# Kernel optimization log

Hardware: AMD Instinct MI355X
Metric: run time of the kernel (lower is better)

Reference implementation:

```python
import jax, jax.numpy as jnp
import numpy as np

D = 1024   # hidden_size
H = 16     # n_head
K = 64     # head_size
B = 4
T = 1024
LAYER_ID = 12
NUM_LAYERS = 24
D_MIX = 32
D_DECAY = 64


def setup_inputs() -> dict:
    key = jax.random.key(0)
    ks = jax.random.split(key, 12)
    r01 = LAYER_ID / (NUM_LAYERS - 1)          # ratio_0_to_1
    r10 = 1.0 - LAYER_ID / NUM_LAYERS          # ratio_1_to_almost0
    ddd = jnp.arange(D, dtype=jnp.float32) / D
    maa = lambda p: (1.0 - ddd ** p).reshape(1, 1, D)
    inp = {}
    inp['x'] = jax.random.normal(ks[0], (B, T, D), jnp.float32)
    inp['time_maa_x'] = maa(r10)
    inp['time_maa_w'] = maa(r10)
    inp['time_maa_k'] = maa(r10)
    inp['time_maa_v'] = (1.0 - (ddd ** r10 + 0.3 * r01)).reshape(1, 1, D)
    inp['time_maa_r'] = maa(0.5 * r10)
    inp['time_maa_g'] = maa(0.5 * r10)
    # torch inits time_maa_w1 to zeros (trivial); use small uniform like w2 for a non-degenerate test
    inp['time_maa_w1'] = jax.random.uniform(ks[1], (D, D_MIX * 5), jnp.float32, -0.01, 0.01)
    inp['time_maa_w2'] = jax.random.uniform(ks[2], (5, D_MIX, D), jnp.float32, -0.01, 0.01)
    n = jnp.arange(D, dtype=jnp.float32)
    inp['time_decay'] = (-6.0 + 5.0 * (n / (D - 1)) ** (0.7 + 1.3 * r01)).reshape(1, 1, D)
    inp['time_decay_w1'] = jax.random.uniform(ks[3], (D, D_DECAY), jnp.float32, -0.01, 0.01)
    inp['time_decay_w2'] = jax.random.uniform(ks[4], (D_DECAY, D), jnp.float32, -0.01, 0.01)
    for nm, kk in zip(['W_r', 'W_k', 'W_v', 'W_g', 'W_o'], ks[5:10]):
        inp[nm] = jax.random.normal(kk, (D, D), jnp.float32) * 0.02
    inp['ln_w'] = jnp.ones((D,), jnp.float32)
    inp['ln_b'] = jnp.zeros((D,), jnp.float32)
    return inp


def _bidir_shift(x):
    # (x[i-1] + x[i+1]) / 2 with zero padding at the boundaries
    left = jnp.pad(x[:, :-1, :], ((0, 0), (1, 0), (0, 0)))
    right = jnp.pad(x[:, 1:, :], ((0, 0), (0, 1), (0, 0)))
    return 0.5 * (left + right)


def _lion_attention(r, k, v, w):
    # r,k,v,w: (B,H,T,Khd), w = -exp(decay) <= 0
    Tn = r.shape[2]
    cs = jnp.cumsum(w, axis=2)
    cs_b = cs - w
    shift_f = cs[:, :, Tn // 2:Tn // 2 + 1, :]
    shift_b = cs_b[:, :, Tn // 2:Tn // 2 + 1, :]
    cf = jnp.clip(cs - shift_f, -60.0, 60.0)
    cb = jnp.clip(cs_b - shift_b, -60.0, 60.0)
    # A_fwd = tril(Q*e^{cf} @ (K*e^{-cf})^T); A_bwd = triu(Q*e^{-cb} @ (K*e^{cb})^T, 1)
    A_f = jnp.einsum('bhik,bhjk->bhij', r * jnp.exp(cf), k * jnp.exp(-cf))
    A_b = jnp.einsum('bhik,bhjk->bhij', r * jnp.exp(-cb), k * jnp.exp(cb))
    idx = jnp.arange(Tn)
    lower = idx[:, None] >= idx[None, :]   # tril incl. diagonal
    A = jnp.where(lower, A_f, A_b)         # == tril(A_f) + triu(A_b, 1)
    return jnp.einsum('bhij,bhjk->bhik', A, v)


def reference(x, time_maa_x, time_maa_w, time_maa_k, time_maa_v, time_maa_r, time_maa_g,
              time_maa_w1, time_maa_w2, time_decay, time_decay_w1, time_decay_w2,
              W_r, W_k, W_v, W_g, W_o, ln_w, ln_b):
    Bn, Tn, Dn = x.shape
    Hh, Kk = H, Dn // H
    dxprev = _bidir_shift(x) - x
    # data-dependent token-shift mixing coefficients (LoRA-style)
    xxx = jnp.tanh((x + dxprev * time_maa_x) @ time_maa_w1)          # (B,T,5*32)
    mm = jnp.einsum('btfm,fmd->fbtd', xxx.reshape(Bn, Tn, 5, D_MIX), time_maa_w2)
    mw, mk, mv, mr, mg = mm[0], mm[1], mm[2], mm[3], mm[4]
    xw = x + dxprev * (time_maa_w + mw)
    xk = x + dxprev * (time_maa_k + mk)
    xv = x + dxprev * (time_maa_v + mv)
    xr = x + dxprev * (time_maa_r + mr)
    xg = x + dxprev * (time_maa_g + mg)
    r = xr @ W_r.T
    k = xk @ W_k.T
    v = xv @ W_v.T
    g = jax.nn.silu(xg @ W_g.T)
    w = time_decay + jnp.tanh(xw @ time_decay_w1) @ time_decay_w2   # (B,T,D)
    to_h = lambda t: t.reshape(Bn, Tn, Hh, Kk).transpose(0, 2, 1, 3)
    y = _lion_attention(to_h(r), to_h(k), to_h(v), -jnp.exp(to_h(w)))
    y = y.transpose(0, 2, 1, 3).reshape(Bn * Tn, Dn)
    # GroupNorm(n_head groups, eps = 1e-5 * head_size_divisor^2)
    eps = 1e-5 * 64.0
    yg = y.reshape(Bn * Tn, Hh, Kk)
    mu = jnp.mean(yg, axis=-1, keepdims=True)
    var = jnp.var(yg, axis=-1, keepdims=True)
    yn = ((yg - mu) * jax.lax.rsqrt(var + eps)).reshape(Bn * Tn, Dn) * ln_w + ln_b
    y = yn.reshape(Bn, Tn, Dn)
    return (y * g) @ W_o.T
```

## Files before the change

### kernel.cpp

```cpp
#include <hip/hip_runtime.h>
#include <math.h>

#define NB 4
#define TT 1024
#define DD 1024
#define NTOK 4096
#define ND (NTOK*DD)

typedef __attribute__((ext_vector_type(8))) short bh8;
typedef __attribute__((ext_vector_type(4))) float fx4;

__device__ __forceinline__ unsigned short f2bf(float f) {
    unsigned int b = __float_as_uint(f);
    b += 0x7fffu + ((b >> 16) & 1u);
    return (unsigned short)(b >> 16);
}

__device__ __forceinline__ unsigned pkbf(float a, float b) {
#if __has_builtin(__builtin_amdgcn_cvt_pk_bf16_f32)
    auto r = __builtin_amdgcn_cvt_pk_bf16_f32(a, b);
    unsigned u;
    __builtin_memcpy(&u, &r, 4);
    return u;
#else
    return ((unsigned)f2bf(b) << 16) | f2bf(a);
#endif
}

#define GLD16(gp, lp) __builtin_amdgcn_global_load_lds( \
    (__attribute__((address_space(1))) void*)(gp), \
    (__attribute__((address_space(3))) void*)(lp), 16, 0, 0)

__global__ __launch_bounds__(256) void k_prep(const float* __restrict__ W_r, const float* __restrict__ W_k,
                                              const float* __restrict__ W_v, const float* __restrict__ W_g,
                                              const float* __restrict__ W_o,
                                              const float* __restrict__ w1, const float* __restrict__ dw1,
                                              const float* __restrict__ w2,
                                              unsigned short* __restrict__ Wrb, unsigned short* __restrict__ Wkb,
                                              unsigned short* __restrict__ Wvb, unsigned short* __restrict__ Wgb,
                                              unsigned short* __restrict__ Wob,
                                              unsigned short* __restrict__ w1T, unsigned short* __restrict__ dw1T,
                                              unsigned short* __restrict__ w2T16) {
    int y = blockIdx.y, bx = blockIdx.x, tid = threadIdx.x;
    if (y < 5) {
        if (bx >= 512) return;
        const float* s = (y == 0) ? W_r : (y == 1) ? W_k : (y == 2) ? W_v : (y == 3) ? W_g : W_o;
        unsigned short* d = (y == 0) ? Wrb : (y == 1) ? Wkb : (y == 2) ? Wvb : (y == 3) ? Wgb : Wob;
        int i = (bx * 256 + tid) * 8;
        float4 a = *(const float4*)(s + i);
        float4 b = *(const float4*)(s + i + 4);
        uint4 o;
        o.x = pkbf(a.x, a.y);
        o.y = pkbf(a.z, a.w);
        o.z = pkbf(b.x, b.y);
        o.w = pkbf(b.z, b.w);
        *(uint4*)(d + i) = o;
    } else if (y == 5) {
        int o = bx * 256 + tid;
        int r = o & 1023, c = o >> 10;
        w1T[o] = f2bf(w1[r * 160 + c]);
    } else {
        if (bx < 256) {
            int o = bx * 256 + tid;
            int r = o & 1023, c = o >> 10;
            dw1T[o] = f2bf(dw1[r * 64 + c]);
        } else if (bx < 276) {
            int wi = bx - 256;
            int f = wi >> 2;
            int d = (wi & 3) * 256 + tid;
#pragma unroll 8
            for (int m = 0; m < 32; m++)
                w2T16[(size_t)(f * 1024 + d) * 32 + m] = f2bf(w2[(size_t)(f * 32 + m) * 1024 + d]);
        }
    }
}

__global__ __launch_bounds__(256) void k_mixx(const float* __restrict__ x,
                                              const float* __restrict__ maa_x,
                                              unsigned short* __restrict__ xmix16) {
    int base = (blockIdx.x * 256 + threadIdx.x) * 4;
    int t = (base >> 10) & 1023;
    int d = base & 1023;
    float4 xv = *(const float4*)(x + base);
    float4 xm = (t > 0)    ? *(const float4*)(x + base - 1024) : make_float4(0, 0, 0, 0);
// ... 150 lines not shown
    for (int c = 0; c < 4; c++) {
        int d = c * 256 + tid;
        float acc[8] = {};
#pragma unroll 8
        for (int j = 0; j < 64; j++) {
            float wv = dw2[j * 1024 + d];
#pragma unroll
            for (int g = 0; g < 8; g++) acc[g] = fmaf(hl[g][j], wv, acc[g]);
        }
        float td = tdec[d];
#pragma unroll
        for (int g = 0; g < 8; g++) ew[(tok0 + g) * 1024 + d] = -expf(td + acc[g]);
    }
}

__global__ __launch_bounds__(64) void k_scan1(const float* __restrict__ ew, float* __restrict__ segsum) {
    int bx = blockIdx.x;
    int b = bx >> 9, seg = (bx >> 4) & 31, dch = bx & 15;
    int d = dch * 64 + threadIdx.x;
    size_t base = ((size_t)(b * 1024 + seg * 32)) * 1024 + d;
    float s = 0.f;
#pragma unroll 8
    for (int t = 0; t < 32; t++) s += ew[base + (size_t)t * 1024];
    segsum[(b * 32 + seg) * 1024 + d] = s;
}

__global__ __launch_bounds__(64) void k_scan3(const float* __restrict__ ew, const float* __restrict__ segsum,
                                              float* __restrict__ cf, float* __restrict__ cb) {
    int bx = blockIdx.x;
    int b = bx >> 9, seg = (bx >> 4) & 31, dch = bx & 15;
    int d = dch * 64 + threadIdx.x;
    float run = 0.f, pre = 0.f, off16 = 0.f;
#pragma unroll
    for (int s = 0; s < 32; s++) {
        float tv = segsum[(b * 32 + s) * 1024 + d];
        if (s == seg) pre = run;
        if (s == 16) off16 = run;
        run += tv;
    }
    float e512 = ew[((size_t)(b * 1024 + 512)) * 1024 + d];
    float sb = off16;
    float sf = off16 + e512;
    float cum = pre;
    size_t base = ((size_t)(b * 1024 + seg * 32)) * 1024 + d;
#pragma unroll 4
    for (int t = 0; t < 32; t++) {
        float prev = cum;
        cum += ew[base + (size_t)t * 1024];
        cf[base + (size_t)t * 1024] = fminf(fmaxf(cum - sf, -60.f), 60.f);
        cb[base + (size_t)t * 1024] = fminf(fmaxf(prev - sb, -60.f), 60.f);
    }
}

__device__ __forceinline__ void gemm_body(const unsigned short* __restrict__ A,
                                          const unsigned short* __restrict__ W,
                                          int m0, int n0, int mode,
                                          float* __restrict__ Cf,
                                          unsigned short* __restrict__ O1,
                                          unsigned short* __restrict__ O2,
                                          const float* __restrict__ cfp,
                                          const float* __restrict__ cbp,
                                          char* smem) {
    int tid = threadIdx.x;
    int w = tid >> 6, lane = tid & 63, l15 = lane & 15, qd = lane >> 4;
    int wm = w >> 1, wn = w & 1;
    fx4 acc[4][4];
#pragma unroll
    for (int mt = 0; mt < 4; mt++)
#pragma unroll
        for (int nt = 0; nt < 4; nt++)
#pragma unroll
            for (int r = 0; r < 4; r++) acc[mt][nt][r] = 0.f;
    unsigned short* sA = (unsigned short*)smem;
    unsigned short* sB = (unsigned short*)(smem + 8192);
    int rowA = tid >> 2, cA = tid & 3;
    for (int kb = 0; kb < 1024; kb += 32) {
        __syncthreads();
        GLD16(A + (size_t)(m0 + rowA) * 1024 + kb + cA * 8,      sA + w * 512);
        GLD16(A + (size_t)(m0 + 64 + rowA) * 1024 + kb + cA * 8, sA + 2048 + w * 512);
        GLD16(W + (size_t)(n0 + rowA) * 1024 + kb + cA * 8,      sB + w * 512);
        GLD16(W + (size_t)(n0 + 64 + rowA) * 1024 + kb + cA * 8, sB + 2048 + w * 512);
        __syncthreads();
        bh8 af[4], bfr[4];
#pragma unroll
        for (int mt = 0; mt < 4; mt++)
            af[mt] = *(const bh8*)(sA + (wm * 64 + mt * 16 + l15) * 32 + qd * 8);
#pragma unroll
        for (int nt = 0; nt < 4; nt++)
            bfr[nt] = *(const bh8*)(sB + (wn * 64 + nt * 16 + l15) * 32 + qd * 8);
#pragma unroll
        for (int mt = 0; mt < 4; mt++)
#pragma unroll
            for (int nt = 0; nt < 4; nt++)
                acc[mt][nt] = __builtin_amdgcn_mfma_f32_16x16x32_bf16(af[mt], bfr[nt], acc[mt][nt], 0, 0, 0);
    }
    int mb = m0 + wm * 64, nb = n0 + wn * 64;
    if (mode <= 1) {
#pragma unroll
        for (int mt = 0; mt < 4; mt++)
#pragma unroll
            for (int nt = 0; nt < 4; nt++) {
                fx4 s = acc[mt][nt];
#pragma unroll
                for (int r = 0; r < 4; r++) {
                    float v = s[r];
                    if (mode == 1) v = v / (1.f + __expf(-v));
                    Cf[(size_t)(mb + mt * 16 + qd * 4 + r) * 1024 + nb + nt * 16 + l15] = v;
                }
            }
    } else if (mode <= 3) {
        float s1 = (mode == 2) ? 1.f : -1.f;
#pragma unroll
        for (int mt = 0; mt < 4; mt++)
#pragma unroll
            for (int nt = 0; nt < 4; nt++) {
                fx4 s = acc[mt][nt];
#pragma unroll
                for (int r = 0; r < 4; r++) {
                    size_t idx = (size_t)(mb + mt * 16 + qd * 4 + r) * 1024 + nb + nt * 16 + l15;
                    float v = s[r];
                    O1[idx] = f2bf(v * __expf(s1 * cfp[idx]));
                    O2[idx] = f2bf(v * __expf(-s1 * cbp[idx]));
                }
            }
    } else {
        __syncthreads();
        unsigned short* T = (unsigned short*)smem;
#pragma unroll
        for (int mt = 0; mt < 4; mt++)
#pragma unroll
            for (int nt = 0; nt < 4; nt++) {
                fx4 s = acc[mt][nt];
                int dl = wn * 64 + nt * 16 + l15;
                int tl = wm * 64 + mt * 16 + qd * 4;
                uint2 pk;
                pk.x = pkbf(s[0], s[1]);
                pk.y = pkbf(s[2], s[3]);
                *(uint2*)(T + dl * 136 + tl) = pk;
            }
        __syncthreads();
        int dl = tid >> 1, hf = tid & 1;
        int bq = m0 >> 10, t0 = m0 & 1023;
#pragma unroll
        for (int i = 0; i < 8; i++) {
            uint4 vv4 = *(const uint4*)(T + dl * 136 + hf * 64 + i * 8);
            *(uint4*)(O1 + (size_t)(bq * 1024 + n0 + dl) * 1024 + t0 + hf * 64 + i * 8) = vv4;
        }
    }
}

__global__ __launch_bounds__(256, 2) void k_gemm4(const unsigned short* __restrict__ xr16,
                                                  const unsigned short* __restrict__ xk16,
                                                  const unsigned short* __restrict__ xv16,
                                                  const unsigned short* __restrict__ xg16,
                                                  const unsigned short* __restrict__ Wrb,
                                                  const unsigned short* __restrict__ Wkb,
                                                  const unsigned short* __restrict__ Wvb,
                                                  const unsigned short* __restrict__ Wgb,
                                                  unsigned short* __restrict__ qf, unsigned short* __restrict__ qb,
                                                  unsigned short* __restrict__ kf, unsigned short* __restrict__ kb,
                                                  unsigned short* __restrict__ vvt,
                                                  float* __restrict__ gg,
                                                  const float* __restrict__ cf, const float* __restrict__ cb) {
    __shared__ __align__(16) char smem[34816];
    int m0 = (blockIdx.x >> 3) * 128, n0 = (blockIdx.x & 7) * 128;
    int y = blockIdx.y;
    if (y == 0)      gemm_body(xr16, Wrb, m0, n0, 2, nullptr, qf, qb, cf, cb, smem);
    else if (y == 1) gemm_body(xk16, Wkb, m0, n0, 3, nullptr, kf, kb, cf, cb, smem);
    else if (y == 2) gemm_body(xv16, Wvb, m0, n0, 4, nullptr, vvt, nullptr, nullptr, nullptr, smem);
    else             gemm_body(xg16, Wgb, m0, n0, 1, gg, nullptr, nullptr, nullptr, nullptr, smem);
}

__global__ __launch_bounds__(256, 2) void k_gemmo(const unsigned short* __restrict__ z16,
                                                  const unsigned short* __restrict__ Wob,
                                                  float* __restrict__ out) {
    __shared__ __align__(16) char smem[34816];
    gemm_body(z16, Wob, (blockIdx.x >> 3) * 128, (blockIdx.x & 7) * 128, 0, out,
              nullptr, nullptr, nullptr, nullptr, smem);
}

__global__ __launch_bounds__(256, 2) void k_attn(const unsigned short* __restrict__ qf,
                                                 const unsigned short* __restrict__ qb,
                                                 const unsigned short* __restrict__ kf,
                                                 const unsigned short* __restrict__ kb,
                                                 const unsigned short* __restrict__ vvt,
                                                 float* __restrict__ y) {
    __shared__ __align__(16) char smem[16384];
    unsigned short* sK = (unsigned short*)smem;
    unsigned short* sV = (unsigned short*)(smem + 8192);
    int tid = threadIdx.x;
    int w = tid >> 6, lane = tid & 63, l15 = lane & 15, qd = lane >> 4;
    int bid = blockIdx.x;
    int bh = (bid & 7) + ((bid >> 6) << 3);
    int ib = (bid >> 3) & 7;
    int b = bh >> 4, h = bh & 15;
    int i0w = ib * 128 + w * 32;
    int bt0 = b * 1024;
    const unsigned short* vrow = vvt + (size_t)(b * 1024 + h * 64 + w * 16 + l15) * 1024 + qd * 8;
    int fmax = (i0w + 31) >> 6;
    int bmin = i0w >> 6;
    int srcA = l15 + ((lane & 16) << 1);
    int srcB = srcA + 16;
    fx4 yacc[4][2];
#pragma unroll
    for (int mt = 0; mt < 4; mt++)
#pragma unroll
        for (int nt = 0; nt < 2; nt++)
#pragma unroll
            for (int r = 0; r < 4; r++) yacc[mt][nt][r] = 0.f;

    for (int phase = 0; phase < 2; phase++) {
        const unsigned short* Q = phase ? qb : qf;
        const unsigned short* K = phase ? kb : kf;
        bh8 qfr[2][2];
#pragma unroll
        for (int nt = 0; nt < 2; nt++)
#pragma unroll
            for (int ks = 0; ks < 2; ks++)
                qfr[nt][ks] = *(const bh8*)(Q + (size_t)(bt0 + i0w + nt * 16 + l15) * 1024
                                              + h * 64 + ks * 32 + qd * 8);
        int jlo = phase == 0 ? 0 : 2 * ib;
        int jhi = phase == 0 ? 2 * ib + 1 : 15;
        const unsigned short* krow = K + (size_t)(bt0 + w * 16 + l15) * 1024 + h * 64 + qd * 8;
        for (int jt = jlo; jt <= jhi; jt++) {
            int jb = jt * 64;
            __syncthreads();
            GLD16(krow + (size_t)jb * 1024,        sK + w * 512);
            GLD16(krow + (size_t)jb * 1024 + 32,   sK + 2048 + w * 512);
            GLD16(vrow + jb,                        sV + w * 512);
            GLD16(vrow + jb + 32,                   sV + 2048 + w * 512);
            __syncthreads();
// ... 116 lines not shown
    const float* dw1   = (const float*)d_in[10];
    const float* dw2   = (const float*)d_in[11];
    const float* W_r   = (const float*)d_in[12];
    const float* W_k   = (const float*)d_in[13];
    const float* W_v   = (const float*)d_in[14];
    const float* W_g   = (const float*)d_in[15];
    const float* W_o   = (const float*)d_in[16];
    const float* lnw   = (const float*)d_in[17];
    const float* lnb   = (const float*)d_in[18];

    float* ws = (float*)d_ws;
    size_t o = 0;
    float* dech   = ws + o; o += 262144;
    float* segsum = ws + o; o += 131072;
    float* ew     = ws + o; o += 4194304;
    float* cf     = ws + o; o += 4194304;
    float* cb     = ws + o; o += 4194304;
    float* gg     = ws + o; o += 4194304;
    unsigned short* us = (unsigned short*)(ws + o);
    size_t u = 0;
    unsigned short* xmix16 = us + u; u += 4194304;
    unsigned short* xw16 = us + u; u += 4194304;
    unsigned short* xr16 = us + u; u += 4194304;
    unsigned short* xk16 = us + u; u += 4194304;
    unsigned short* xv16 = us + u; u += 4194304;
    unsigned short* xg16 = us + u; u += 4194304;
    unsigned short* qf   = us + u; u += 4194304;
    unsigned short* qb   = us + u; u += 4194304;
    unsigned short* kf   = us + u; u += 4194304;
    unsigned short* kb   = us + u; u += 4194304;
    unsigned short* vvt  = us + u; u += 4194304;
    unsigned short* Wrb  = us + u; u += 1048576;
    unsigned short* Wkb  = us + u; u += 1048576;
    unsigned short* Wvb  = us + u; u += 1048576;
    unsigned short* Wgb  = us + u; u += 1048576;
    unsigned short* Wob  = us + u; u += 1048576;
    unsigned short* w1T  = us + u; u += 163840;
    unsigned short* dw1T = us + u; u += 65536;
    unsigned short* xxx16 = us + u; u += 655360;
    unsigned short* w2T16 = us + u; u += 163840;
    float* yb0 = cf;
    unsigned short* z16 = xr16;

    k_prep<<<dim3(640, 7), 256, 0, stream>>>(W_r, W_k, W_v, W_g, W_o, w1, dw1, w2,
                                             Wrb, Wkb, Wvb, Wgb, Wob, w1T, dw1T, w2T16);
    k_mixx<<<4096, 256, 0, stream>>>(x, maa_x, xmix16);
    k_xxx2<<<256, 64, 0, stream>>>(xmix16, w1T, xxx16);
    k_mmix<<<dim3(16, 32), 256, 0, stream>>>(x, xxx16, w2T16, maa_w, maa_k, maa_v, maa_r, maa_g,
                                             xw16, xk16, xv16, xr16, xg16);
    k_dec1m<<<256, 64, 0, stream>>>(xw16, dw1T, dech);
    k_dec2<<<512, 256, 0, stream>>>(dech, dw2, tdec, ew);
    k_scan1<<<2048, 64, 0, stream>>>(ew, segsum);
    k_scan3<<<2048, 64, 0, stream>>>(ew, segsum, cf, cb);
    k_gemm4<<<dim3(256, 4), 256, 0, stream>>>(xr16, xk16, xv16, xg16, Wrb, Wkb, Wvb, Wgb,
                                              qf, qb, kf, kb, vvt, gg, cf, cb);
    k_attn<<<512, 256, 0, stream>>>(qf, qb, kf, kb, vvt, yb0);
    k_gn<<<16384, 256, 0, stream>>>(yb0, gg, lnw, lnb, z16);
    k_gemmo<<<256, 256, 0, stream>>>(z16, Wob, (float*)d_out);
}
```

Before: 344.8 us.

## Replace QKVG GEMM with 256x256-tile double-buffered 512-thread pipelined kernel

Replaces the 128x128-tile four-way GEMM for r/k/v/g projections with a new kernel using 256x256 tiles, 512 threads, and 128KB of LDS double-buffered via direct global-to-LDS loads. The K loop is split into phases that interleave async loads with MFMA bursts under raised wave priority, with an XCD-aware block remap. It aims to raise arithmetic intensity and overlap memory with compute. The cost is lower occupancy, since 128KB of LDS allows one block per CU despite the launch bound, and a more fragile hand-tuned waitcnt schedule.

```diff
diff --git a/kernel.cpp b/kernel.cpp
--- a/kernel.cpp
+++ b/kernel.cpp
@@ -30,6 +30,8 @@
 #define GLD16(gp, lp) __builtin_amdgcn_global_load_lds( \
     (__attribute__((address_space(1))) void*)(gp), \
     (__attribute__((address_space(3))) void*)(lp), 16, 0, 0)
+
+#define BARF() do { __builtin_amdgcn_s_barrier(); asm volatile("" ::: "memory"); } while (0)
 
 __global__ __launch_bounds__(256) void k_prep(const float* __restrict__ W_r, const float* __restrict__ W_k,
                                               const float* __restrict__ W_v, const float* __restrict__ W_g,
@@ -383,26 +385,176 @@
     }
 }
 
-__global__ __launch_bounds__(256, 2) void k_gemm4(const unsigned short* __restrict__ xr16,
-                                                  const unsigned short* __restrict__ xk16,
-                                                  const unsigned short* __restrict__ xv16,
-                                                  const unsigned short* __restrict__ xg16,
-                                                  const unsigned short* __restrict__ Wrb,
-                                                  const unsigned short* __restrict__ Wkb,
-                                                  const unsigned short* __restrict__ Wvb,
-                                                  const unsigned short* __restrict__ Wgb,
-                                                  unsigned short* __restrict__ qf, unsigned short* __restrict__ qb,
-                                                  unsigned short* __restrict__ kf, unsigned short* __restrict__ kb,
-                                                  unsigned short* __restrict__ vvt,
-                                                  float* __restrict__ gg,
-                                                  const float* __restrict__ cf, const float* __restrict__ cb) {
-    __shared__ __align__(16) char smem[34816];
-    int m0 = (blockIdx.x >> 3) * 128, n0 = (blockIdx.x & 7) * 128;
-    int y = blockIdx.y;
-    if (y == 0)      gemm_body(xr16, Wrb, m0, n0, 2, nullptr, qf, qb, cf, cb, smem);
-    else if (y == 1) gemm_body(xk16, Wkb, m0, n0, 3, nullptr, kf, kb, cf, cb, smem);
-    else if (y == 2) gemm_body(xv16, Wvb, m0, n0, 4, nullptr, vvt, nullptr, nullptr, nullptr, smem);
-    else             gemm_body(xg16, Wgb, m0, n0, 1, gg, nullptr, nullptr, nullptr, nullptr, smem);
+
+#define STA(dstbuf, g, kbv, Apt) GLD16(Apt + (size_t)(m0 + aBase + (g) * 32 + lr) * 1024 + (kbv) + swz, \
+                                       (dstbuf) + (aBase + (g) * 32) * 64)
+#define STB(dstbuf, s, kbv, Wpt) GLD16(Wpt + (size_t)(n0 + bBase + (s) * 64 + lr) * 1024 + (kbv) + swz, \
+                                       (dstbuf) + (bBase + (s) * 64) * 64)
+
+#define PHASE(mt0_, STAGE_, TAIL_) do {                                                  \
+    bh8 aA0 = *(const bh8*)(sAc + arA + (mt0_) * 1024 + fc0);                            \
+    bh8 aA1 = *(const bh8*)(sAc + arA + (mt0_) * 1024 + fc1);                            \
+    bh8 aB0 = *(const bh8*)(sAc + arA + ((mt0_) + 1) * 1024 + fc0);                      \
+    bh8 aB1 = *(const bh8*)(sAc + arA + ((mt0_) + 1) * 1024 + fc1);                      \
+    STAGE_;                                                                              \
+    BARF();                                                                              \
+    asm volatile("s_waitcnt lgkmcnt(0)" ::: "memory");                                   \
+    __builtin_amdgcn_s_setprio(1);                                                       \
+    _Pragma("unroll")                                                                    \
+    for (int nt = 0; nt < 4; ++nt) {                                                     \
+        acc[(mt0_)][nt]     = __builtin_amdgcn_mfma_f32_16x16x32_bf16(aA0, bfr[nt][0], acc[(mt0_)][nt], 0, 0, 0);     \
+        acc[(mt0_)][nt]     = __builtin_amdgcn_mfma_f32_16x16x32_bf16(aA1, bfr[nt][1], acc[(mt0_)][nt], 0, 0, 0);     \
+        acc[(mt0_) + 1][nt] = __builtin_amdgcn_mfma_f32_16x16x32_bf16(aB0, bfr[nt][0], acc[(mt0_) + 1][nt], 0, 0, 0); \
+        acc[(mt0_) + 1][nt] = __builtin_amdgcn_mfma_f32_16x16x32_bf16(aB1, bfr[nt][1], acc[(mt0_) + 1][nt], 0, 0, 0); \
+    }                                                                                    \
+    __builtin_amdgcn_s_setprio(0);                                                       \
+    TAIL_;                                                                               \
+    BARF();                                                                              \
+} while (0)
+
+__global__ __launch_bounds__(512, 2) void k_qkvg(const unsigned short* __restrict__ xr16,
+                                                 const unsigned short* __restrict__ xk16,
+                                                 const unsigned short* __restrict__ xv16,
+                                                 const unsigned short* __restrict__ xg16,
+                                                 const unsigned short* __restrict__ Wrb,
+                                                 const unsigned short* __restrict__ Wkb,
+                                                 const unsigned short* __restrict__ Wvb,
+                                                 const unsigned short* __restrict__ Wgb,
+                                                 unsigned short* __restrict__ qf, unsigned short* __restrict__ qb,
+                                                 unsigned short* __restrict__ kf, unsigned short* __restrict__ kb,
+                                                 unsigned short* __restrict__ vvt,
+                                                 float* __restrict__ gg,
+                                                 const float* __restrict__ cf, const float* __restrict__ cb) {
+    __shared__ __align__(16) char smem[131072];
+    unsigned short* sA0 = (unsigned short*)smem;
+    unsigned short* sB0 = (unsigned short*)(smem + 32768);
+    unsigned short* sA1 = (unsigned short*)(smem + 65536);
+    unsigned short* sB1 = (unsigned short*)(smem + 98304);
+
+    int flat = blockIdx.x;
+    int wk = (flat & 7) * 32 + (flat >> 3);
+    int gy = wk >> 6;
+    int wi = wk & 63;
+    int m0 = (wi >> 2) * 256, n0 = (wi & 3) * 256;
+
+    const unsigned short* Ap = (gy == 0) ? xr16 : (gy == 1) ? xk16 : (gy == 2) ? xv16 : xg16;
+    const unsigned short* Wp = (gy == 0) ? Wrb : (gy == 1) ? Wkb : (gy == 2) ? Wvb : Wgb;
+
+    int tid = threadIdx.x;
+    int lane = tid & 63, w = tid >> 6;
+    int l15 = lane & 15, qd = lane >> 4;
+    int wm = w >> 2, wn = w & 3;
+    int lr = lane >> 3;
+    int swz = ((lane & 7) ^ lr) << 3;
+    int aBase = wm * 128 + (w & 3) * 8;
+    int bBase = w * 8;
+    int fc0 = (qd * 8) ^ ((l15 & 7) << 3);
+    int fc1 = fc0 ^ 32;
+    int arA = (wm * 128 + l15) * 64;
+    int arB = (wn * 64 + l15) * 64;
+
+    fx4 acc[8][4];
+#pragma unroll
+    for (int mt = 0; mt < 8; mt++)
+#pragma unroll
+        for (int nt = 0; nt < 4; nt++)
+#pragma unroll
+            for (int r = 0; r < 4; r++) acc[mt][nt][r] = 0.f;
+
+#pragma unroll
+    for (int g = 0; g < 4; ++g) STA(sA0, g, 0, Ap);
+#pragma unroll
+    for (int s = 0; s < 4; ++s) STB(sB0, s, 0, Wp);
+    asm volatile("" ::: "memory");
+#pragma unroll
+    for (int s = 0; s < 4; ++s) STB(sB1, s, 64, Wp);
+    STA(sA1, 0, 64, Ap);
+    STA(sA1, 1, 64, Ap);
+    asm volatile("s_waitcnt vmcnt(6)" ::: "memory");
+    BARF();
+
+    unsigned short* sAc = sA0;
+    unsigned short* sBc = sB0;
+    unsigned short* sAn = sA1;
+    unsigned short* sBn = sB1;
+
+#pragma unroll 1
+    for (int t = 0; t < 16; ++t) {
+        int kb1 = t * 64 + 64, kb2 = t * 64 + 128;
+        bh8 bfr[4][2];
+#pragma unroll
+        for (int nt = 0; nt < 4; ++nt) {
+            bfr[nt][0] = *(const bh8*)(sBc + arB + nt * 1024 + fc0);
+            bfr[nt][1] = *(const bh8*)(sBc + arB + nt * 1024 + fc1);
+        }
+        PHASE(0, if (t < 15) { STA(sAn, 2, kb1, Ap); STA(sAn, 3, kb1, Ap); }, );
+        PHASE(2, if (t < 14) { STB(sBc, 0, kb2, Wp); STB(sBc, 1, kb2, Wp); }, );
+        PHASE(4, if (t < 14) { STB(sBc, 2, kb2, Wp); STB(sBc, 3, kb2, Wp); }, );
+        PHASE(6, if (t < 14) { STA(sAc, 0, kb2, Ap); STA(sAc, 1, kb2, Ap); },
+                 if (t < 14) { asm volatile("s_waitcnt vmcnt(6)" ::: "memory"); }
+                 else if (t == 14) { asm volatile("s_waitcnt vmcnt(0)" ::: "memory"); } );
+        unsigned short* tp;
+        tp = sAc; sAc = sAn; sAn = tp;
+        tp = sBc; sBc = sBn; sBn = tp;
+    }
+
+    int mb = m0 + wm * 128, nb = n0 + wn * 64;
+    if (gy == 3) {
+#pragma unroll
+        for (int mt = 0; mt < 8; mt++)
+#pragma unroll
+            for (int nt = 0; nt < 4; nt++)
+#pragma unroll
+                for (int r = 0; r < 4; r++) {
+                    float v = acc[mt][nt][r];
+                    v = v / (1.f + __expf(-v));
+                    gg[(size_t)(mb + mt * 16 + qd * 4 + r) * 1024 + nb + nt * 16 + l15] = v;
+                }
+    } else if (gy == 2) {
+        __syncthreads();
+        unsigned short* T = (unsigned short*)smem;
+        int bq = m0 >> 10, t0 = m0 & 1023;
+#pragma unroll 1
+        for (int h = 0; h < 2; ++h) {
+            if (wm == h) {
+#pragma unroll
+                for (int mt = 0; mt < 8; mt++)
+#pragma unroll
+                    for (int nt = 0; nt < 4; nt++) {
+                        int dl = wn * 64 + nt * 16 + l15;
+                        int rl = mt * 16 + qd * 4;
+                        uint2 pk;
+                        pk.x = pkbf(acc[mt][nt][0], acc[mt][nt][1]);
+                        pk.y = pkbf(acc[mt][nt][2], acc[mt][nt][3]);
+                        *(uint2*)(T + dl * 136 + rl) = pk;
+                    }
+            }
+            __syncthreads();
+#pragma unroll
+            for (int i = 0; i < 8; ++i) {
+                int gch = i * 512 + tid;
+                int d = gch >> 4, tch = gch & 15;
+                uint4 vv = *(const uint4*)(T + d * 136 + tch * 8);
+                *(uint4*)(vvt + (size_t)(bq * 1024 + n0 + d) * 1024 + t0 + h * 128 + tch * 8) = vv;
+            }
+            __syncthreads();
+        }
+    } else {
+        unsigned short* O1 = gy ? kf : qf;
+        unsigned short* O2 = gy ? kb : qb;
+        float s1 = gy ? -1.f : 1.f;
+#pragma unroll
+        for (int mt = 0; mt < 8; mt++)
+#pragma unroll
+            for (int nt = 0; nt < 4; nt++)
+#pragma unroll
+                for (int r = 0; r < 4; r++) {
+                    size_t idx = (size_t)(mb + mt * 16 + qd * 4 + r) * 1024 + nb + nt * 16 + l15;
+                    float v = acc[mt][nt][r];
+                    O1[idx] = f2bf(v * __expf(s1 * cf[idx]));
+                    O2[idx] = f2bf(v * __expf(-s1 * cb[idx]));
+                }
+    }
 }
 
 __global__ __launch_bounds__(256, 2) void k_gemmo(const unsigned short* __restrict__ z16,
@@ -633,8 +785,8 @@
     k_dec2<<<512, 256, 0, stream>>>(dech, dw2, tdec, ew);
     k_scan1<<<2048, 64, 0, stream>>>(ew, segsum);
     k_scan3<<<2048, 64, 0, stream>>>(ew, segsum, cf, cb);
-    k_gemm4<<<dim3(256, 4), 256, 0, stream>>>(xr16, xk16, xv16, xg16, Wrb, Wkb, Wvb, Wgb,
-                                              qf, qb, kf, kb, vvt, gg, cf, cb);
+    k_qkvg<<<dim3(256), dim3(512), 0, stream>>>(xr16, xk16, xv16, xg16, Wrb, Wkb, Wvb, Wgb,
+                                                qf, qb, kf, kb, vvt, gg, cf, cb);
     k_attn<<<512, 256, 0, stream>>>(qf, qb, kf, kb, vvt, yb0);
     k_gn<<<16384, 256, 0, stream>>>(yb0, gg, lnw, lnb, z16);
     k_gemmo<<<256, 256, 0, stream>>>(z16, Wob, (float*)d_out);
```

Measured after the change: 343.7 us. Within noise of the previous version (-0.3%).

## Replace QKVG GEMM with 128x256-tile, 512-thread, triple-buffered direct-to-LDS kernel

Applied to the files above, without the earlier changes.

The four projection GEMMs move from the shared gemm_body (128x128 tiles, 256 threads) to a dedicated kernel with 128x256 tiles, 8 waves, and a three-stage global_load_lds pipeline using explicit vmcnt waits and raw barriers. Block indices are remapped so that consecutive blocks are spread across XCDs. MFMA sections are wrapped in s_setprio. The epilogues for silu, the decay-scaled q/k outputs and the transposed v are rewritten to fit the new tiling. The goal is more reuse per loaded tile and better overlap of memory with compute, at the cost of a 72KB LDS footprint per block that limits occupancy.

```diff
diff --git a/kernel.cpp b/kernel.cpp
--- a/kernel.cpp
+++ b/kernel.cpp
@@ -30,6 +30,8 @@
 #define GLD16(gp, lp) __builtin_amdgcn_global_load_lds( \
     (__attribute__((address_space(1))) void*)(gp), \
     (__attribute__((address_space(3))) void*)(lp), 16, 0, 0)
+
+#define BARF() do { __builtin_amdgcn_s_barrier(); asm volatile("" ::: "memory"); } while (0)
 
 __global__ __launch_bounds__(256) void k_prep(const float* __restrict__ W_r, const float* __restrict__ W_k,
                                               const float* __restrict__ W_v, const float* __restrict__ W_g,
@@ -383,26 +385,155 @@
     }
 }
 
-__global__ __launch_bounds__(256, 2) void k_gemm4(const unsigned short* __restrict__ xr16,
-                                                  const unsigned short* __restrict__ xk16,
-                                                  const unsigned short* __restrict__ xv16,
-                                                  const unsigned short* __restrict__ xg16,
-                                                  const unsigned short* __restrict__ Wrb,
-                                                  const unsigned short* __restrict__ Wkb,
-                                                  const unsigned short* __restrict__ Wvb,
-                                                  const unsigned short* __restrict__ Wgb,
-                                                  unsigned short* __restrict__ qf, unsigned short* __restrict__ qb,
-                                                  unsigned short* __restrict__ kf, unsigned short* __restrict__ kb,
-                                                  unsigned short* __restrict__ vvt,
-                                                  float* __restrict__ gg,
-                                                  const float* __restrict__ cf, const float* __restrict__ cb) {
-    __shared__ __align__(16) char smem[34816];
-    int m0 = (blockIdx.x >> 3) * 128, n0 = (blockIdx.x & 7) * 128;
-    int y = blockIdx.y;
-    if (y == 0)      gemm_body(xr16, Wrb, m0, n0, 2, nullptr, qf, qb, cf, cb, smem);
-    else if (y == 1) gemm_body(xk16, Wkb, m0, n0, 3, nullptr, kf, kb, cf, cb, smem);
-    else if (y == 2) gemm_body(xv16, Wvb, m0, n0, 4, nullptr, vvt, nullptr, nullptr, nullptr, smem);
-    else             gemm_body(xg16, Wgb, m0, n0, 1, gg, nullptr, nullptr, nullptr, nullptr, smem);
+__global__ __launch_bounds__(512, 2) void k_qkvg(const unsigned short* __restrict__ xr16,
+                                                 const unsigned short* __restrict__ xk16,
+                                                 const unsigned short* __restrict__ xv16,
+                                                 const unsigned short* __restrict__ xg16,
+                                                 const unsigned short* __restrict__ Wrb,
+                                                 const unsigned short* __restrict__ Wkb,
+                                                 const unsigned short* __restrict__ Wvb,
+                                                 const unsigned short* __restrict__ Wgb,
+                                                 unsigned short* __restrict__ qf, unsigned short* __restrict__ qb,
+                                                 unsigned short* __restrict__ kf, unsigned short* __restrict__ kb,
+                                                 unsigned short* __restrict__ vvt,
+                                                 float* __restrict__ gg,
+                                                 const float* __restrict__ cf, const float* __restrict__ cb) {
+    __shared__ __align__(16) char smem[73728];
+    int flat = blockIdx.x;
+    int wk = (flat & 7) * 64 + (flat >> 3);
+    int gy = wk >> 7;
+    int rem = wk & 127;
+    int m0 = (rem >> 2) * 128, n0 = (rem & 3) * 256;
+
+    const unsigned short* Ap = (gy == 0) ? xr16 : (gy == 1) ? xk16 : (gy == 2) ? xv16 : xg16;
+    const unsigned short* Wp = (gy == 0) ? Wrb : (gy == 1) ? Wkb : (gy == 2) ? Wvb : Wgb;
+
+    int tid = threadIdx.x;
+    int lane = tid & 63, w = tid >> 6;
+    int l15 = lane & 15, qd = lane >> 4;
+    int wm = w >> 2, wn = w & 3;
+
+    int lrow = lane >> 2, lblk = lane & 3;
+    int gblk = lblk ^ (lrow & 3);
+    const unsigned short* agp  = Ap + (size_t)(m0 + w * 16 + lrow) * 1024 + gblk * 8;
+    const unsigned short* bgp0 = Wp + (size_t)(n0 + w * 16 + lrow) * 1024 + gblk * 8;
+    const unsigned short* bgp1 = Wp + (size_t)(n0 + 128 + w * 16 + lrow) * 1024 + gblk * 8;
+
+    unsigned short* pa0 = (unsigned short*)smem;
+    unsigned short* pa1 = pa0 + 4096;
+    unsigned short* pa2 = pa0 + 8192;
+    unsigned short* pb0 = (unsigned short*)(smem + 24576);
+    unsigned short* pb1 = pb0 + 8192;
+    unsigned short* pb2 = pb0 + 16384;
+
+    int acb = (qd ^ (l15 & 3)) * 8;
+    int arow = (wm * 64 + l15) * 32;
+    int brow = (wn * 64 + l15) * 32;
+
+#define QSTAGE(pa, pb, kbv) do { \
+    GLD16(agp + (kbv),  (pa) + w * 512); \
+    GLD16(bgp0 + (kbv), (pb) + w * 512); \
+    GLD16(bgp1 + (kbv), (pb) + 4096 + w * 512); \
+} while (0)
+
+    fx4 acc[4][4];
+#pragma unroll
+    for (int mt = 0; mt < 4; mt++)
+#pragma unroll
+        for (int nt = 0; nt < 4; nt++)
+#pragma unroll
+            for (int r = 0; r < 4; r++) acc[mt][nt][r] = 0.f;
+
+    QSTAGE(pa0, pb0, 0);
+    QSTAGE(pa1, pb1, 32);
+    asm volatile("s_waitcnt vmcnt(3)" ::: "memory");
+    BARF();
+
+    unsigned short *pac = pa0, *pan = pa1, *pap = pa2;
+    unsigned short *pbc = pb0, *pbn = pb1, *pbp = pb2;
+
+#pragma unroll 1
+    for (int t = 0; t < 32; ++t) {
+        bh8 a[4], b[4];
+#pragma unroll
+        for (int mt = 0; mt < 4; ++mt) a[mt] = *(const bh8*)(pac + arow + mt * 512 + acb);
+#pragma unroll
+        for (int nt = 0; nt < 4; ++nt) b[nt] = *(const bh8*)(pbc + brow + nt * 512 + acb);
+        if (t < 30) QSTAGE(pap, pbp, (t + 2) * 32);
+        __builtin_amdgcn_s_setprio(1);
+#pragma unroll
+        for (int nt = 0; nt < 4; ++nt)
+#pragma unroll
+            for (int mt = 0; mt < 4; ++mt)
+                acc[mt][nt] = __builtin_amdgcn_mfma_f32_16x16x32_bf16(a[mt], b[nt], acc[mt][nt], 0, 0, 0);
+        __builtin_amdgcn_s_setprio(0);
+        if (t < 30)      asm volatile("s_waitcnt vmcnt(3)" ::: "memory");
+        else if (t == 30) asm volatile("s_waitcnt vmcnt(0)" ::: "memory");
+        BARF();
+        unsigned short* tp;
+        tp = pac; pac = pan; pan = pap; pap = tp;
+        tp = pbc; pbc = pbn; pbn = pbp; pbp = tp;
+    }
+#undef QSTAGE
+
+    int mb = m0 + wm * 64, nb = n0 + wn * 64;
+    if (gy == 3) {
+#pragma unroll
+        for (int mt = 0; mt < 4; mt++)
+#pragma unroll
+            for (int nt = 0; nt < 4; nt++)
+#pragma unroll
+                for (int r = 0; r < 4; r++) {
+                    float v = acc[mt][nt][r];
+                    v = v / (1.f + __expf(-v));
+                    gg[(size_t)(mb + mt * 16 + qd * 4 + r) * 1024 + nb + nt * 16 + l15] = v;
+                }
+    } else if (gy == 2) {
+        __syncthreads();
+        unsigned short* T = (unsigned short*)smem;
+        int bq = m0 >> 10, t0 = m0 & 1023;
+#pragma unroll 1
+        for (int h = 0; h < 2; ++h) {
+            if ((wn >> 1) == h) {
+#pragma unroll
+                for (int mt = 0; mt < 4; mt++)
+#pragma unroll
+                    for (int nt = 0; nt < 4; nt++) {
+                        int dl = (wn & 1) * 64 + nt * 16 + l15;
+                        int tl = wm * 64 + mt * 16 + qd * 4;
+                        uint2 pk;
+                        pk.x = pkbf(acc[mt][nt][0], acc[mt][nt][1]);
+                        pk.y = pkbf(acc[mt][nt][2], acc[mt][nt][3]);
+                        *(uint2*)(T + dl * 136 + tl) = pk;
+                    }
+            }
+            __syncthreads();
+            {
+                int r = tid >> 2, seg = tid & 3;
+#pragma unroll
+                for (int i = 0; i < 4; ++i) {
+                    uint4 vv = *(const uint4*)(T + r * 136 + seg * 32 + i * 8);
+                    *(uint4*)(vvt + (size_t)(bq * 1024 + n0 + 128 * h + r) * 1024 + t0 + seg * 32 + i * 8) = vv;
+                }
+            }
+            __syncthreads();
+        }
+    } else {
+        unsigned short* O1 = gy ? kf : qf;
+        unsigned short* O2 = gy ? kb : qb;
+        float s1 = gy ? -1.f : 1.f;
+#pragma unroll
+        for (int mt = 0; mt < 4; mt++)
+#pragma unroll
+            for (int nt = 0; nt < 4; nt++)
+#pragma unroll
+                for (int r = 0; r < 4; r++) {
+                    size_t idx = (size_t)(mb + mt * 16 + qd * 4 + r) * 1024 + nb + nt * 16 + l15;
+                    float v = acc[mt][nt][r];
+                    O1[idx] = f2bf(v * __expf(s1 * cf[idx]));
+                    O2[idx] = f2bf(v * __expf(-s1 * cb[idx]));
+                }
+    }
 }
 
 __global__ __launch_bounds__(256, 2) void k_gemmo(const unsigned short* __restrict__ z16,
@@ -633,8 +764,8 @@
     k_dec2<<<512, 256, 0, stream>>>(dech, dw2, tdec, ew);
     k_scan1<<<2048, 64, 0, stream>>>(ew, segsum);
     k_scan3<<<2048, 64, 0, stream>>>(ew, segsum, cf, cb);
-    k_gemm4<<<dim3(256, 4), 256, 0, stream>>>(xr16, xk16, xv16, xg16, Wrb, Wkb, Wvb, Wgb,
-                                              qf, qb, kf, kb, vvt, gg, cf, cb);
+    k_qkvg<<<dim3(512), dim3(512), 0, stream>>>(xr16, xk16, xv16, xg16, Wrb, Wkb, Wvb, Wgb,
+                                                qf, qb, kf, kb, vvt, gg, cf, cb);
     k_attn<<<512, 256, 0, stream>>>(qf, qb, kf, kb, vvt, yb0);
     k_gn<<<16384, 256, 0, stream>>>(yb0, gg, lnw, lnb, z16);
     k_gemmo<<<256, 256, 0, stream>>>(z16, Wob, (float*)d_out);
```

Result: no change. 347.2 us (+0.7%).

## Rewrite projection GEMMs with split-K waves, triple-buffered LDS and swizzled tiles

Applied to the files above, without the earlier changes.

Replaces the 128x128 single-buffered GEMM body with a 256x128 tile computed by 8 waves. The waves split K into two halves and reduce their partial sums through LDS. K-tiles of 64 are triple-buffered with direct global-to-LDS loads, manual vmcnt waits and XOR-swizzled layouts, and MFMA priority is raised, all to overlap loads with compute and avoid bank conflicts. Block indices are remapped for L2 locality. The cost is large LDS use (144KB), which limits occupancy to one block per CU, plus an extra reduction pass, and the V-transpose epilogue now runs in two halves.

```diff
diff --git a/kernel.cpp b/kernel.cpp
--- a/kernel.cpp
+++ b/kernel.cpp
@@ -30,6 +30,8 @@
 #define GLD16(gp, lp) __builtin_amdgcn_global_load_lds( \
     (__attribute__((address_space(1))) void*)(gp), \
     (__attribute__((address_space(3))) void*)(lp), 16, 0, 0)
+
+#define BARF() do { __builtin_amdgcn_s_barrier(); asm volatile("" ::: "memory"); } while (0)
 
 __global__ __launch_bounds__(256) void k_prep(const float* __restrict__ W_r, const float* __restrict__ W_k,
                                               const float* __restrict__ W_v, const float* __restrict__ W_g,
@@ -286,131 +288,218 @@
     }
 }
 
-__device__ __forceinline__ void gemm_body(const unsigned short* __restrict__ A,
-                                          const unsigned short* __restrict__ W,
-                                          int m0, int n0, int mode,
-                                          float* __restrict__ Cf,
-                                          unsigned short* __restrict__ O1,
-                                          unsigned short* __restrict__ O2,
-                                          const float* __restrict__ cfp,
-                                          const float* __restrict__ cbp,
-                                          char* smem) {
+#define QST(slotoff, kbv) do { \
+    unsigned short* _sa = (unsigned short*)(smem + (slotoff)); \
+    unsigned short* _sb = _sa + 16384; \
+    GLD16(aSrc + (kbv),         _sa + (w * 32) * 64); \
+    GLD16(aSrc + 8192 + (kbv),  _sa + (w * 32 + 8) * 64); \
+    GLD16(aSrc + 16384 + (kbv), _sa + (w * 32 + 16) * 64); \
+    GLD16(aSrc + 24576 + (kbv), _sa + (w * 32 + 24) * 64); \
+    GLD16(bSrc + (kbv),         _sb + (w * 16) * 64); \
+    GLD16(bSrc + 8192 + (kbv),  _sb + (w * 16 + 8) * 64); \
+} while (0)
+
+__device__ __forceinline__ void gemm_k2(const unsigned short* __restrict__ A,
+                                        const unsigned short* __restrict__ W,
+                                        int m0, int n0, int mode,
+                                        float* __restrict__ Cf,
+                                        unsigned short* __restrict__ O1,
+                                        unsigned short* __restrict__ O2,
+                                        const float* __restrict__ cfp,
+                                        const float* __restrict__ cbp,
+                                        char* smem) {
     int tid = threadIdx.x;
-    int w = tid >> 6, lane = tid & 63, l15 = lane & 15, qd = lane >> 4;
-    int wm = w >> 1, wn = w & 1;
-    fx4 acc[4][4];
-#pragma unroll
-    for (int mt = 0; mt < 4; mt++)
+    int lane = tid & 63, w = tid >> 6;
+    int l15 = lane & 15, qd = lane >> 4;
+    int wk = w >> 2, wm = (w >> 1) & 1, wn = w & 1;
+    int lr = lane >> 3, lb = lane & 7;
+    int gblk = lb ^ lr;
+    const unsigned short* aSrc = A + (size_t)(m0 + w * 32 + lr) * 1024 + gblk * 8;
+    const unsigned short* bSrc = W + (size_t)(n0 + w * 16 + lr) * 1024 + gblk * 8;
+    int fc = ((wk * 4 + qd) ^ (l15 & 7)) * 8;
+    int arow = (wm * 128 + l15) * 64 + fc;
+    int brow = (wn * 64 + l15) * 64 + fc;
+
+    fx4 acc[8][4];
+#pragma unroll
+    for (int mt = 0; mt < 8; mt++)
 #pragma unroll
         for (int nt = 0; nt < 4; nt++)
 #pragma unroll
             for (int r = 0; r < 4; r++) acc[mt][nt][r] = 0.f;
-    unsigned short* sA = (unsigned short*)smem;
-    unsigned short* sB = (unsigned short*)(smem + 8192);
-    int rowA = tid >> 2, cA = tid & 3;
-    for (int kb = 0; kb < 1024; kb += 32) {
-        __syncthreads();
-        GLD16(A + (size_t)(m0 + rowA) * 1024 + kb + cA * 8,      sA + w * 512);
-        GLD16(A + (size_t)(m0 + 64 + rowA) * 1024 + kb + cA * 8, sA + 2048 + w * 512);
-        GLD16(W + (size_t)(n0 + rowA) * 1024 + kb + cA * 8,      sB + w * 512);
-        GLD16(W + (size_t)(n0 + 64 + rowA) * 1024 + kb + cA * 8, sB + 2048 + w * 512);
-        __syncthreads();
-        bh8 af[4], bfr[4];
-#pragma unroll
-        for (int mt = 0; mt < 4; mt++)
-            af[mt] = *(const bh8*)(sA + (wm * 64 + mt * 16 + l15) * 32 + qd * 8);
-#pragma unroll
-        for (int nt = 0; nt < 4; nt++)
-            bfr[nt] = *(const bh8*)(sB + (wn * 64 + nt * 16 + l15) * 32 + qd * 8);
-#pragma unroll
-        for (int mt = 0; mt < 4; mt++)
-#pragma unroll
-            for (int nt = 0; nt < 4; nt++)
-                acc[mt][nt] = __builtin_amdgcn_mfma_f32_16x16x32_bf16(af[mt], bfr[nt], acc[mt][nt], 0, 0, 0);
-    }
-    int mb = m0 + wm * 64, nb = n0 + wn * 64;
-    if (mode <= 1) {
-#pragma unroll
-        for (int mt = 0; mt < 4; mt++)
-#pragma unroll
-            for (int nt = 0; nt < 4; nt++) {
-                fx4 s = acc[mt][nt];
-#pragma unroll
-                for (int r = 0; r < 4; r++) {
-                    float v = s[r];
-                    if (mode == 1) v = v / (1.f + __expf(-v));
-                    Cf[(size_t)(mb + mt * 16 + qd * 4 + r) * 1024 + nb + nt * 16 + l15] = v;
-                }
-            }
-    } else if (mode <= 3) {
-        float s1 = (mode == 2) ? 1.f : -1.f;
-#pragma unroll
-        for (int mt = 0; mt < 4; mt++)
-#pragma unroll
-            for (int nt = 0; nt < 4; nt++) {
-                fx4 s = acc[mt][nt];
-#pragma unroll
-                for (int r = 0; r < 4; r++) {
-                    size_t idx = (size_t)(mb + mt * 16 + qd * 4 + r) * 1024 + nb + nt * 16 + l15;
-                    float v = s[r];
-                    O1[idx] = f2bf(v * __expf(s1 * cfp[idx]));
-                    O2[idx] = f2bf(v * __expf(-s1 * cbp[idx]));
-                }
+
+    QST(0, 0);
+    QST(49152, 64);
+    asm volatile("s_waitcnt vmcnt(6)" ::: "memory");
+    BARF();
+
+    int oc = 0, on = 49152, o2 = 98304;
+#pragma unroll 1
+    for (int t = 0; t < 16; ++t) {
+        if (t < 14) QST(o2, (t + 2) * 64);
+        const unsigned short* cA = (const unsigned short*)(smem + oc);
+        const unsigned short* cB = cA + 16384;
+        bh8 a[8], b[4];
+#pragma unroll
+        for (int mt = 0; mt < 8; ++mt) a[mt] = *(const bh8*)(cA + arow + mt * 1024);
+#pragma unroll
+        for (int nt = 0; nt < 4; ++nt) b[nt] = *(const bh8*)(cB + brow + nt * 1024);
+        __builtin_amdgcn_s_setprio(1);
+#pragma unroll
+        for (int nt = 0; nt < 4; ++nt)
+#pragma unroll
+            for (int mt = 0; mt < 8; ++mt)
+                acc[mt][nt] = __builtin_amdgcn_mfma_f32_16x16x32_bf16(a[mt], b[nt], acc[mt][nt], 0, 0, 0);
+        __builtin_amdgcn_s_setprio(0);
+        asm volatile("s_waitcnt lgkmcnt(0)" ::: "memory");
+        if (t < 14)       asm volatile("s_waitcnt vmcnt(6)" ::: "memory");
+        else if (t == 14) asm volatile("s_waitcnt vmcnt(0)" ::: "memory");
+        BARF();
+        int tmp = oc; oc = on; on = o2; o2 = tmp;
+    }
+
+    float* R = (float*)smem;
+    float* rb = R + (wm * 2 + wn) * 8192 + lane * 4;
+    if (wk == 1) {
+#pragma unroll
+        for (int mi = 0; mi < 4; ++mi)
+#pragma unroll
+            for (int nt = 0; nt < 4; ++nt)
+                *(fx4*)(rb + (mi * 4 + nt) * 256) = acc[mi][nt];
+    } else {
+#pragma unroll
+        for (int mi = 0; mi < 4; ++mi)
+#pragma unroll
+            for (int nt = 0; nt < 4; ++nt)
+                *(fx4*)(rb + (16 + mi * 4 + nt) * 256) = acc[mi + 4][nt];
+    }
+    asm volatile("s_waitcnt lgkmcnt(0)" ::: "memory");
+    BARF();
+    if (wk == 0) {
+#pragma unroll
+        for (int mi = 0; mi < 4; ++mi)
+#pragma unroll
+            for (int nt = 0; nt < 4; ++nt) {
+                fx4 v = *(const fx4*)(rb + (mi * 4 + nt) * 256);
+                acc[mi][nt] = acc[mi][nt] + v;
             }
     } else {
-        __syncthreads();
+#pragma unroll
+        for (int mi = 0; mi < 4; ++mi)
+#pragma unroll
+            for (int nt = 0; nt < 4; ++nt) {
+                fx4 v = *(const fx4*)(rb + (16 + mi * 4 + nt) * 256);
+                acc[mi + 4][nt] = acc[mi + 4][nt] + v;
+            }
+    }
+    asm volatile("s_waitcnt lgkmcnt(0)" ::: "memory");
+    BARF();
+
+    int mbase = m0 + wm * 128;
+    int nb = n0 + wn * 64;
+#define EPI(AOFF) do { \
+    if (mode <= 1) { \
+        _Pragma("unroll") \
+        for (int mi = 0; mi < 4; ++mi) \
+        { _Pragma("unroll") \
+          for (int nt = 0; nt < 4; ++nt) \
+          { _Pragma("unroll") \
+            for (int r = 0; r < 4; ++r) { \
+                float v = acc[mi + AOFF][nt][r]; \
+                if (mode == 1) v = v / (1.f + __expf(-v)); \
+                Cf[(size_t)(mbase + (mi + AOFF) * 16 + qd * 4 + r) * 1024 + nb + nt * 16 + l15] = v; \
+            } } } \
+    } else if (mode <= 3) { \
+        float s1 = (mode == 2) ? 1.f : -1.f; \
+        _Pragma("unroll") \
+        for (int mi = 0; mi < 4; ++mi) \
+        { _Pragma("unroll") \
+          for (int nt = 0; nt < 4; ++nt) \
+          { _Pragma("unroll") \
+            for (int r = 0; r < 4; ++r) { \
+                size_t idx = (size_t)(mbase + (mi + AOFF) * 16 + qd * 4 + r) * 1024 + nb + nt * 16 + l15; \
+                float v = acc[mi + AOFF][nt][r]; \
+                O1[idx] = f2bf(v * __expf(s1 * cfp[idx])); \
+                O2[idx] = f2bf(v * __expf(-s1 * cbp[idx])); \
+            } } } \
+    } \
+} while (0)
+    if (mode != 4) {
+        if (wk == 0) EPI(0); else EPI(4);
+    } else {
         unsigned short* T = (unsigned short*)smem;
-#pragma unroll
-        for (int mt = 0; mt < 4; mt++)
-#pragma unroll
-            for (int nt = 0; nt < 4; nt++) {
-                fx4 s = acc[mt][nt];
-                int dl = wn * 64 + nt * 16 + l15;
-                int tl = wm * 64 + mt * 16 + qd * 4;
-                uint2 pk;
-                pk.x = pkbf(s[0], s[1]);
-                pk.y = pkbf(s[2], s[3]);
-                *(uint2*)(T + dl * 136 + tl) = pk;
+        int bq = m0 >> 10, t0 = m0 & 1023;
+#define VW(AOFF) do { \
+    _Pragma("unroll") \
+    for (int mi = 0; mi < 4; ++mi) \
+    { _Pragma("unroll") \
+      for (int nt = 0; nt < 4; ++nt) { \
+        int dl = wn * 64 + nt * 16 + l15; \
+        int tl = (mi + AOFF) * 16 + qd * 4; \
+        uint2 pk2; \
+        pk2.x = pkbf(acc[mi + AOFF][nt][0], acc[mi + AOFF][nt][1]); \
+        pk2.y = pkbf(acc[mi + AOFF][nt][2], acc[mi + AOFF][nt][3]); \
+        *(uint2*)(T + dl * 136 + tl) = pk2; \
+    } } \
+} while (0)
+#pragma unroll 1
+        for (int h = 0; h < 2; ++h) {
+            if (wm == h) {
+                if (wk == 0) VW(0); else VW(4);
             }
-        __syncthreads();
-        int dl = tid >> 1, hf = tid & 1;
-        int bq = m0 >> 10, t0 = m0 & 1023;
-#pragma unroll
-        for (int i = 0; i < 8; i++) {
-            uint4 vv4 = *(const uint4*)(T + dl * 136 + hf * 64 + i * 8);
-            *(uint4*)(O1 + (size_t)(bq * 1024 + n0 + dl) * 1024 + t0 + hf * 64 + i * 8) = vv4;
-        }
-    }
-}
-
-__global__ __launch_bounds__(256, 2) void k_gemm4(const unsigned short* __restrict__ xr16,
-                                                  const unsigned short* __restrict__ xk16,
-                                                  const unsigned short* __restrict__ xv16,
-                                                  const unsigned short* __restrict__ xg16,
-                                                  const unsigned short* __restrict__ Wrb,
-                                                  const unsigned short* __restrict__ Wkb,
-                                                  const unsigned short* __restrict__ Wvb,
-                                                  const unsigned short* __restrict__ Wgb,
-                                                  unsigned short* __restrict__ qf, unsigned short* __restrict__ qb,
-                                                  unsigned short* __restrict__ kf, unsigned short* __restrict__ kb,
-                                                  unsigned short* __restrict__ vvt,
-                                                  float* __restrict__ gg,
-                                                  const float* __restrict__ cf, const float* __restrict__ cb) {
-    __shared__ __align__(16) char smem[34816];
-    int m0 = (blockIdx.x >> 3) * 128, n0 = (blockIdx.x & 7) * 128;
-    int y = blockIdx.y;
-    if (y == 0)      gemm_body(xr16, Wrb, m0, n0, 2, nullptr, qf, qb, cf, cb, smem);
-    else if (y == 1) gemm_body(xk16, Wkb, m0, n0, 3, nullptr, kf, kb, cf, cb, smem);
-    else if (y == 2) gemm_body(xv16, Wvb, m0, n0, 4, nullptr, vvt, nullptr, nullptr, nullptr, smem);
-    else             gemm_body(xg16, Wgb, m0, n0, 1, gg, nullptr, nullptr, nullptr, nullptr, smem);
-}
-
-__global__ __launch_bounds__(256, 2) void k_gemmo(const unsigned short* __restrict__ z16,
+            asm volatile("s_waitcnt lgkmcnt(0)" ::: "memory");
+            BARF();
+#pragma unroll
+            for (int i = 0; i < 4; ++i) {
+                int idx = i * 512 + tid;
+                int dd = idx >> 4, u = idx & 15;
+                uint4 vv = *(const uint4*)(T + dd * 136 + u * 8);
+                *(uint4*)(O1 + (size_t)(bq * 1024 + n0 + dd) * 1024 + t0 + h * 128 + u * 8) = vv;
+            }
+            asm volatile("s_waitcnt lgkmcnt(0)" ::: "memory");
+            BARF();
+        }
+#undef VW
+    }
+#undef EPI
+}
+
+__global__ __launch_bounds__(512, 2) void k_qkvg(const unsigned short* __restrict__ xr16,
+                                                 const unsigned short* __restrict__ xk16,
+                                                 const unsigned short* __restrict__ xv16,
+                                                 const unsigned short* __restrict__ xg16,
+                                                 const unsigned short* __restrict__ Wrb,
+                                                 const unsigned short* __restrict__ Wkb,
+                                                 const unsigned short* __restrict__ Wvb,
+                                                 const unsigned short* __restrict__ Wgb,
+                                                 unsigned short* __restrict__ qf, unsigned short* __restrict__ qb,
+                                                 unsigned short* __restrict__ kf, unsigned short* __restrict__ kb,
+                                                 unsigned short* __restrict__ vvt,
+                                                 float* __restrict__ gg,
+                                                 const float* __restrict__ cf, const float* __restrict__ cb) {
+    __shared__ __align__(16) char smem[147456];
+    int flat = blockIdx.x;
+    int wkid = (flat & 7) * 64 + (flat >> 3);
+    int gy = wkid >> 7;
+    int rem = wkid & 127;
+    int m0 = (rem >> 3) * 256, n0 = (rem & 7) * 128;
+    const unsigned short* Ap = (gy == 0) ? xr16 : (gy == 1) ? xk16 : (gy == 2) ? xv16 : xg16;
+    const unsigned short* Wp = (gy == 0) ? Wrb : (gy == 1) ? Wkb : (gy == 2) ? Wvb : Wgb;
+    int mode = (gy == 0) ? 2 : (gy == 1) ? 3 : (gy == 2) ? 4 : 1;
+    unsigned short* o1 = (gy == 0) ? qf : (gy == 1) ? kf : (gy == 2) ? vvt : nullptr;
+    unsigned short* o2 = (gy == 0) ? qb : (gy == 1) ? kb : nullptr;
+    float* cfo = (gy == 3) ? gg : nullptr;
+    gemm_k2(Ap, Wp, m0, n0, mode, cfo, o1, o2, cf, cb, smem);
+}
+
+__global__ __launch_bounds__(512, 2) void k_gemmo(const unsigned short* __restrict__ z16,
                                                   const unsigned short* __restrict__ Wob,
                                                   float* __restrict__ out) {
-    __shared__ __align__(16) char smem[34816];
-    gemm_body(z16, Wob, (blockIdx.x >> 3) * 128, (blockIdx.x & 7) * 128, 0, out,
-              nullptr, nullptr, nullptr, nullptr, smem);
+    __shared__ __align__(16) char smem[147456];
+    int flat = blockIdx.x;
+    int wkid = (flat & 7) * 16 + (flat >> 3);
+    int m0 = (wkid >> 3) * 256, n0 = (wkid & 7) * 128;
+    gemm_k2(z16, Wob, m0, n0, 0, out, nullptr, nullptr, nullptr, nullptr, smem);
 }
 
 __global__ __launch_bounds__(256, 2) void k_attn(const unsigned short* __restrict__ qf,
@@ -633,9 +722,9 @@
     k_dec2<<<512, 256, 0, stream>>>(dech, dw2, tdec, ew);
     k_scan1<<<2048, 64, 0, stream>>>(ew, segsum);
     k_scan3<<<2048, 64, 0, stream>>>(ew, segsum, cf, cb);
-    k_gemm4<<<dim3(256, 4), 256, 0, stream>>>(xr16, xk16, xv16, xg16, Wrb, Wkb, Wvb, Wgb,
-                                              qf, qb, kf, kb, vvt, gg, cf, cb);
+    k_qkvg<<<dim3(512), dim3(512), 0, stream>>>(xr16, xk16, xv16, xg16, Wrb, Wkb, Wvb, Wgb,
+                                                qf, qb, kf, kb, vvt, gg, cf, cb);
     k_attn<<<512, 256, 0, stream>>>(qf, qb, kf, kb, vvt, yb0);
     k_gn<<<16384, 256, 0, stream>>>(yb0, gg, lnw, lnb, z16);
-    k_gemmo<<<256, 256, 0, stream>>>(z16, Wob, (float*)d_out);
-}
+    k_gemmo<<<128, 512, 0, stream>>>(z16, Wob, (float*)d_out);
+}
```

Result: slower. 389.6 us (+13.0%).
